# Optimization experiments

Hardware: AMD Instinct MI355X
Metric: run time of the kernel (lower is better)

Reference implementation:

```python
import jax, jax.numpy as jnp
import numpy as np

N, M, D_IN, H1, D, OUT_C = 2048, 128, 352, 512, 256, 13


def _lin_bn_relu(x, w, b, g, be):
    # 1x1 conv == linear over last dim; BN (eval) folded to per-channel affine (g, be)
    return jax.nn.relu(g * (x @ w.T + b) + be)


def _encode(x, wA, bA, gA, beA, wB, bB, gB, beB):
    return _lin_bn_relu(_lin_bn_relu(x, wA, bA, gA, beA), wB, bB, gB, beB)


def setup_inputs() -> dict:
    key = jax.random.key(0)
    ks = iter(jax.random.split(key, 64))

    def wgt(shape, s=0.05):
        return (jax.random.normal(next(ks), shape, jnp.float32) * s)

    def gamma(c):
        return 1.0 + 0.05 * jax.random.normal(next(ks), (c,), jnp.float32)

    inp = {}
    inp['ext_fea'] = jax.random.normal(next(ks), (N, D_IN), jnp.float32)
    inp['lab_fea'] = jax.random.normal(next(ks), (M, D_IN), jnp.float32)
    # convs1: 352->512->256, each Conv1d(1x1)+BN+ReLU
    inp.update(w1a=wgt((H1, D_IN)), b1a=wgt((H1,)), g1a=gamma(H1), be1a=wgt((H1,)))
    inp.update(w1b=wgt((D, H1)), b1b=wgt((D,)), g1b=gamma(D), be1b=wgt((D,)))
    # convs2: same shapes
    inp.update(w2a=wgt((H1, D_IN)), b2a=wgt((H1,)), g2a=gamma(H1), be2a=wgt((H1,)))
    inp.update(w2b=wgt((D, H1)), b2b=wgt((D,)), g2b=gamma(D), be2b=wgt((D,)))
    # wei_conv SharedMLP [256,32,64,256]: three Conv2d(1x1)+BN+ReLU
    inp.update(mw1=wgt((32, D)), mb1=wgt((32,)), mg1=gamma(32), mbe1=wgt((32,)))
    inp.update(mw2=wgt((64, 32)), mb2=wgt((64,)), mg2=gamma(64), mbe2=wgt((64,)))
    inp.update(mw3=wgt((D, 64)), mb3=wgt((D,)), mg3=gamma(D), mbe3=wgt((D,)))
    # fc
    inp.update(fcw=wgt((OUT_C, D)), fcb=wgt((OUT_C,)))
    return inp


def reference(ext_fea, lab_fea,
              w1a, b1a, g1a, be1a, w1b, b1b, g1b, be1b,
              w2a, b2a, g2a, be2a, w2b, b2b, g2b, be2b,
              mw1, mb1, mg1, mbe1, mw2, mb2, mg2, mbe2, mw3, mb3, mg3, mbe3,
              fcw, fcb):
    A = _encode(ext_fea, w1a, b1a, g1a, be1a, w1b, b1b, g1b, be1b)   # [N, 256]
    B = _encode(lab_fea, w2a, b2a, g2a, be2a, w2b, b2b, g2b, be2b)   # [M, 256]
    diff = A[:, None, :] - B[None, :, :]                             # [N, M, 256]
    h = _lin_bn_relu(diff, mw1, mb1, mg1, mbe1)                      # [N, M, 32]
    h = _lin_bn_relu(h, mw2, mb2, mg2, mbe2)                         # [N, M, 64]
    wei = _lin_bn_relu(h, mw3, mb3, mg3, mbe3)                       # [N, M, 256]
    # torch softmax over dim=-1 of [1,256,N,M] == over M == axis 1 here
    wei = jax.nn.softmax(wei, axis=1)
    att = jnp.sum(wei * diff, axis=1)                                # [N, 256]
    return att @ fcw.T + fcb                                         # [N, 13]
```

## Files before the change

kernel.cpp:

```cpp
#include <hip/hip_runtime.h>
#include <stdint.h>


typedef __attribute__((ext_vector_type(4))) float float4_t;
typedef __attribute__((ext_vector_type(4))) float f32x4;
typedef __attribute__((ext_vector_type(8))) short bf16x8;
typedef __attribute__((ext_vector_type(8))) unsigned short ushort8_t;
typedef unsigned short ushort_t;

__device__ __forceinline__ unsigned short f2b(float f) {
  union { float f; unsigned int i; } v; v.f = f;
  unsigned int x = v.i;
  return (unsigned short)((x + 0x7FFFu + ((x >> 16) & 1u)) >> 16);
}

template<int ISBF>
__device__ __forceinline__ ushort8_t ld8(const void* base, size_t idx) {
  if constexpr (ISBF) {
    return *(const ushort8_t*)((const ushort_t*)base + idx);
  } else {
    const float* p = (const float*)base + idx;
    float4_t v0 = *(const float4_t*)p;
    float4_t v1 = *(const float4_t*)(p + 4);
    ushort8_t u;
    #pragma unroll
    for (int e = 0; e < 4; ++e) { u[e] = f2b(v0[e]); u[4 + e] = f2b(v1[e]); }
    return u;
  }
}

template<int XBF, int WBF, int OUT_BF16>
__global__ __launch_bounds__(256) void enc_mfma(
    const void* __restrict__ XA, const void* __restrict__ WA,
    const float* __restrict__ bA, const float* __restrict__ gA, const float* __restrict__ beA,
    void* __restrict__ YA,
    const void* __restrict__ XB, const void* __restrict__ WB,
    const float* __restrict__ bB, const float* __restrict__ gB, const float* __restrict__ beB,
    void* __restrict__ YB, float* __restrict__ YBT,
    int J, int K, int nbxA)
{
  __shared__ ushort_t Xs[2][32][40];
  __shared__ ushort_t Ws[2][32][40];
  const int bx = blockIdx.x, by = blockIdx.y;
  const void* X; const void* W;
  const float *bb, *gg, *bev; void* Y; int i0, isB;
  if (bx < nbxA) { X = XA; W = WA; bb = bA; gg = gA; bev = beA; Y = YA; i0 = bx * 32; isB = 0; }
  else           { X = XB; W = WB; bb = bB; gg = gB; bev = beB; Y = YB; i0 = (bx - nbxA) * 32; isB = 1; }
  const int j0 = by * 32;
  const int tid = threadIdx.x, w = tid >> 6, lane = tid & 63, lg = lane >> 4, lr = lane & 15;
  const int mt = w >> 1, ct = w & 1;
  const int row = tid >> 2, k8 = (tid & 3) * 8;

  f32x4 acc = f32x4{0.f, 0.f, 0.f, 0.f};

  ushort8_t sv = (row < 32) ? ld8<XBF>(X, (size_t)(i0 + row) * K + k8)
                            : ld8<WBF>(W, (size_t)(j0 + row - 32) * K + k8);
  for (int kt = 0; kt < K; kt += 32) {
    const int buf = (kt >> 5) & 1;
    if (row < 32) *(ushort8_t*)&Xs[buf][row][k8] = sv;
    else          *(ushort8_t*)&Ws[buf][row - 32][k8] = sv;
    __syncthreads();
    if (kt + 32 < K)
      sv = (row < 32) ? ld8<XBF>(X, (size_t)(i0 + row) * K + kt + 32 + k8)
                      : ld8<WBF>(W, (size_t)(j0 + row - 32) * K + kt + 32 + k8);
    bf16x8 af = *(const bf16x8*)&Xs[buf][mt * 16 + lr][lg * 8];
    bf16x8 bf_ = *(const bf16x8*)&Ws[buf][ct * 16 + lr][lg * 8];
    acc = __builtin_amdgcn_mfma_f32_16x16x32_bf16(af, bf_, acc, 0, 0, 0);
  }
  const int c = j0 + ct * 16 + lr;
  const float g = gg[c], bv = bb[c], ev = bev[c];
  #pragma unroll
  for (int r = 0; r < 4; ++r) {
    const int rowo = i0 + mt * 16 + 4 * lg + r;
    float t = fmaxf(g * (acc[r] + bv) + ev, 0.f);
    if (OUT_BF16) ((ushort_t*)Y)[(size_t)rowo * J + c] = f2b(t);
    else {
      ((float*)Y)[(size_t)rowo * J + c] = t;
      if (isB && YBT) YBT[(size_t)c * 128 + rowo] = t;
    }
  }
}

__global__ __launch_bounds__(256) void proj32(
    const float* __restrict__ Aenc, const float* __restrict__ Benc,
    const float* __restrict__ mw1, const float* __restrict__ mb1,
    const float* __restrict__ mg1, const float* __restrict__ mbe1,
    float* __restrict__ PA2, float* __restrict__ PB2, int nbxA,
    const float* __restrict__ mw2, const float* __restrict__ mw3,
    ushort_t* __restrict__ mw2b, ushort_t* __restrict__ mw3b)
{
  __shared__ float ps[4][32];
  const int tid = threadIdx.x, bx = blockIdx.x;
  if (bx >= nbxA + 32) {
    const int g = (bx - nbxA - 32) * 256 + tid;
    const float* s; ushort_t* d; int j;
    if (g < 256) { s = mw2; d = mw2b; j = g; }
    else         { s = mw3; d = mw3b; j = g - 256; }
    float4_t v0 = *(const float4_t*)&s[(size_t)j * 8];
    float4_t v1 = *(const float4_t*)&s[(size_t)j * 8 + 4];
    ushort8_t u;
    #pragma unroll
    for (int e = 0; e < 4; ++e) { u[e] = f2b(v0[e]); u[4 + e] = f2b(v1[e]); }
    *(ushort8_t*)&d[(size_t)j * 8] = u;
    return;
  }
  const float* X; float* P; int n0, wb;
  if (bx < nbxA) { X = Aenc; P = PA2; n0 = bx * 4; wb = 1; }
  else           { X = Benc; P = PB2; n0 = (bx - nbxA) * 4; wb = 0; }
  const int k = tid & 31, r = (tid >> 5) & 3, half = tid >> 7;
  const int n = n0 + r;
  const float* xp = &X[(size_t)n * 256 + half * 128];
  const float* wp = &mw1[k * 256 + half * 128];
  float s = 0.f;
  #pragma unroll 8
  for (int q = 0; q < 128; q += 4) {
    float4_t xv = *(const float4_t*)&xp[q];
    float4_t wv = *(const float4_t*)&wp[q];
    #pragma unroll
    for (int e = 0; e < 4; ++e) s = fmaf(xv[e], wv[e], s);
  }
  if (half == 1) ps[r][k] = s;
  __syncthreads();
  if (half == 0) {
    s += ps[r][k];
    P[(size_t)n * 32 + k] = wb ? (mg1[k] * (s + mb1[k]) + mbe1[k]) : (mg1[k] * s);
  }
}

__global__ __launch_bounds__(256, 2) void main_attn(
    const float* __restrict__ PA2, const float* __restrict__ PB2,
    const float* __restrict__ A, const float* __restrict__ BmT,
    const ushort_t* __restrict__ mw2b, const float* __restrict__ mb2,
    const float* __restrict__ mg2, const float* __restrict__ mbe2,
    const ushort_t* __restrict__ mw3b, const float* __restrict__ mb3,
    const float* __restrict__ mg3, const float* __restrict__ mbe3,
    const float* __restrict__ fcw, const float* __restrict__ fcb,
    float* __restrict__ outp)
{
  __shared__ __align__(16) char smem[77824];
  const int tid = threadIdx.x;
  const int w = tid >> 6, lane = tid & 63, lg = lane >> 4, lr = lane & 15;
  const int n = blockIdx.x * 4 + w;
  ushort_t* h2s = (ushort_t*)(smem + w * 19456);
  float* attL   = (float*)(smem + w * 19456 + 18432);
  const float LOG2E = 1.4426950408889634f;

  {
    bf16x8 b1[4];
    float g2h[4], b2h[4], e2h[4];
    #pragma unroll
    for (int jt = 0; jt < 4; ++jt) {
      b1[jt] = *(const bf16x8*)&mw2b[(jt * 16 + lr) * 32 + lg * 8];
      const int j = jt * 16 + lr;
      g2h[jt] = mg2[j]; b2h[jt] = mb2[j]; e2h[jt] = mbe2[j];
    }
    const float* pa = &PA2[(size_t)n * 32 + lg * 8];
    float4_t pa0 = *(const float4_t*)pa;
    float4_t pa1 = *(const float4_t*)(pa + 4);
    #pragma unroll
    for (int mt = 0; mt < 8; ++mt) {
      const int m = mt * 16 + lr;
      const float* pb = &PB2[(size_t)m * 32 + lg * 8];
      float4_t pb0 = *(const float4_t*)pb;
      float4_t pb1 = *(const float4_t*)(pb + 4);
      bf16x8 a1;
      #pragma unroll
      for (int e = 0; e < 4; ++e) {
        a1[e]     = (short)f2b(fmaxf(pa0[e] - pb0[e], 0.f));
        a1[4 + e] = (short)f2b(fmaxf(pa1[e] - pb1[e], 0.f));
      }
      f32x4 acc1[4];
      #pragma unroll
      for (int jt = 0; jt < 4; ++jt) acc1[jt] = f32x4{0.f, 0.f, 0.f, 0.f};
      #pragma unroll
      for (int jt = 0; jt < 4; ++jt)
        acc1[jt] = __builtin_amdgcn_mfma_f32_16x16x32_bf16(a1, b1[jt], acc1[jt], 0, 0, 0);
      #pragma unroll
      for (int jt = 0; jt < 4; ++jt)
        #pragma unroll
        for (int r = 0; r < 4; ++r)
          h2s[(mt * 16 + 4 * lg + r) * 72 + jt * 16 + lr] =
              f2b(fmaxf(g2h[jt] * (acc1[jt][r] + b2h[jt]) + e2h[jt], 0.f));
    }
  }

  #pragma unroll 2
  for (int ct = 0; ct < 16; ++ct) {
    const int c = ct * 16 + lr;
    bf16x8 bfr0 = *(const bf16x8*)&mw3b[(size_t)c * 64 + lg * 8];
    bf16x8 bfr1 = *(const bf16x8*)&mw3b[(size_t)c * 64 + 32 + lg * 8];
    f32x4 acc[8];
    #pragma unroll
    for (int mt = 0; mt < 8; ++mt) acc[mt] = f32x4{0.f, 0.f, 0.f, 0.f};
    #pragma unroll
    for (int mt = 0; mt < 8; ++mt) {
      bf16x8 af0 = *(const bf16x8*)&h2s[(mt * 16 + lr) * 72 + lg * 8];
      acc[mt] = __builtin_amdgcn_mfma_f32_16x16x32_bf16(af0, bfr0, acc[mt], 0, 0, 0);
      bf16x8 af1 = *(const bf16x8*)&h2s[(mt * 16 + lr) * 72 + 32 + lg * 8];
      acc[mt] = __builtin_amdgcn_mfma_f32_16x16x32_bf16(af1, bfr1, acc[mt], 0, 0, 0);
    }
    const float g = mg3[c];
    const float gs = g * LOG2E;
    const float cs = (g * mb3[c] + mbe3[c]) * LOG2E;
    f32x4 sm4 = f32x4{0.f, 0.f, 0.f, 0.f};
    f32x4 wb4 = f32x4{0.f, 0.f, 0.f, 0.f};
    #pragma unroll
    for (int mt = 0; mt < 8; ++mt) {
      float4_t bv4 = *(const float4_t*)&BmT[(size_t)c * 128 + mt * 16 + 4 * lg];
      #pragma unroll
      for (int r = 0; r < 4; ++r) {
        float t = fmaf(gs, acc[mt][r], cs);
        float p = __builtin_amdgcn_exp2f(__builtin_amdgcn_fmed3f(t, 0.f, 80.f));
        sm4[r] += p;
        wb4[r] = fmaf(p, bv4[r], wb4[r]);
      }
    }
    float sm = (sm4[0] + sm4[1]) + (sm4[2] + sm4[3]);
    float wb = (wb4[0] + wb4[1]) + (wb4[2] + wb4[3]);
    sm += __shfl_xor(sm, 16, 64);  wb += __shfl_xor(wb, 16, 64);
    sm += __shfl_xor(sm, 32, 64);  wb += __shfl_xor(wb, 32, 64);
    if (lg == 0)
      attL[c] = A[(size_t)n * 256 + c] - wb / sm;
  }

  {
    float4_t av = *(const float4_t*)&attL[lane * 4];
    #pragma unroll
    for (int o = 0; o < 13; ++o) {
      float4_t wv = *(const float4_t*)&fcw[(size_t)o * 256 + lane * 4];
      float s = av[0] * wv[0];
      s = fmaf(av[1], wv[1], s);
      s = fmaf(av[2], wv[2], s);
      s = fmaf(av[3], wv[3], s);
      #pragma unroll
      for (int st = 1; st <= 32; st <<= 1) s += __shfl_xor(s, st, 64);
      if (lane == 0) outp[(size_t)n * 13 + o] = s + fcb[o];
    }
  }
}

extern "C" void kernel_launch(void* const* d_in, const int* in_sizes, int n_in,
                              void* d_out, int out_size, void* d_ws, size_t ws_size,
                              hipStream_t stream)
{
  const float* ext = (const float*)d_in[0];
  const float* lab = (const float*)d_in[1];
  const float* w1a = (const float*)d_in[2];
  const float* b1a = (const float*)d_in[3];
  const float* g1a = (const float*)d_in[4];
  const float* be1a= (const float*)d_in[5];
  const float* w1b = (const float*)d_in[6];
  const float* b1b = (const float*)d_in[7];
  const float* g1b = (const float*)d_in[8];
  const float* be1b= (const float*)d_in[9];
  const float* w2a = (const float*)d_in[10];
  const float* b2a = (const float*)d_in[11];
  const float* g2a = (const float*)d_in[12];
  const float* be2a= (const float*)d_in[13];
  const float* w2b = (const float*)d_in[14];
  const float* b2b = (const float*)d_in[15];
  const float* g2b = (const float*)d_in[16];
  const float* be2b= (const float*)d_in[17];
  const float* mw1 = (const float*)d_in[18];
  const float* mb1 = (const float*)d_in[19];
  const float* mg1 = (const float*)d_in[20];
  const float* mbe1= (const float*)d_in[21];
  const float* mw2 = (const float*)d_in[22];
  const float* mb2 = (const float*)d_in[23];
  const float* mg2 = (const float*)d_in[24];
  const float* mbe2= (const float*)d_in[25];
  const float* mw3 = (const float*)d_in[26];
  const float* mb3 = (const float*)d_in[27];
  const float* mg3 = (const float*)d_in[28];
  const float* mbe3= (const float*)d_in[29];
  const float* fcw = (const float*)d_in[30];
  const float* fcb = (const float*)d_in[31];

  char* ws = (char*)d_ws;
  ushort_t* Y1ab = (ushort_t*)(ws);
  float*    PA2  = (float*)(ws);
  float*    PB2  = (float*)(ws + 262144);
  float*    Aenc = (float*)(ws + (2u << 20));
  char* b5 = ws + (4u << 20);
  ushort_t* mw2b = (ushort_t*)(b5);
  ushort_t* mw3b = (ushort_t*)(b5 + 4096);
  ushort_t* Y1bb = (ushort_t*)(b5 + 36864);
  float*    Benc = (float*)(b5 + 167936);
  float*    BencT= (float*)(b5 + 299008);

  enc_mfma<0, 0, 1><<<dim3(68, 16), 256, 0, stream>>>(
      (const void*)ext, (const void*)w1a, b1a, g1a, be1a, (void*)Y1ab,
      (const void*)lab, (const void*)w2a, b2a, g2a, be2a, (void*)Y1bb,
      (float*)nullptr, 512, 352, 64);
  enc_mfma<1, 0, 0><<<dim3(68, 8), 256, 0, stream>>>(
      (const void*)Y1ab, (const void*)w1b, b1b, g1b, be1b, (void*)Aenc,
      (const void*)Y1bb, (const void*)w2b, b2b, g2b, be2b, (void*)Benc,
      BencT, 256, 512, 64);
  proj32<<<553, 256, 0, stream>>>(Aenc, Benc, mw1, mb1, mg1, mbe1, PA2, PB2, 512,
                                  mw2, mw3, mw2b, mw3b);
  main_attn<<<512, 256, 0, stream>>>(PA2, PB2, Aenc, BencT,
                                     mw2b, mb2, mg2, mbe2, mw3b, mb3, mg3, mbe3,
                                     fcw, fcb, (float*)d_out);
}
```

Measured before the change: 86.34 us.

## Fold BN scale into mw3 bf16 weights, restructure softmax loop, store B transposed as bf16

Pre-scales the third MLP weight by gamma*log2e during bf16 conversion and seeds the MFMA accumulator with the bias term, so the exponent input comes straight from the matrix product with no per-element affine step. The channel loop is restructured to hold 8 channel tiles' weights in registers and reuse each loaded h2 fragment across them, which cuts LDS reads. The transposed B encoding is stored and read as bf16 to halve its traffic, and a cheaper round-to-nearest bf16 conversion is used in the hot path. The cost is more register pressure and slightly lower precision in the weighted sum and the rounding.

```diff
diff --git a/kernel.cpp b/kernel.cpp
--- a/kernel.cpp
+++ b/kernel.cpp
@@ -6,12 +6,20 @@
 typedef __attribute__((ext_vector_type(4))) float f32x4;
 typedef __attribute__((ext_vector_type(8))) short bf16x8;
 typedef __attribute__((ext_vector_type(8))) unsigned short ushort8_t;
+typedef __attribute__((ext_vector_type(4))) unsigned short ushort4_t;
 typedef unsigned short ushort_t;
 
+__device__ __forceinline__ float b2f(unsigned short u) {
+  union { unsigned int i; float f; } v; v.i = ((unsigned int)u) << 16; return v.f;
+}
 __device__ __forceinline__ unsigned short f2b(float f) {
   union { float f; unsigned int i; } v; v.f = f;
   unsigned int x = v.i;
   return (unsigned short)((x + 0x7FFFu + ((x >> 16) & 1u)) >> 16);
+}
+__device__ __forceinline__ unsigned short f2b_fast(float f) {
+  union { float f; unsigned int i; } v; v.f = f;
+  return (unsigned short)((v.i + 0x8000u) >> 16);
 }
 
 template<int ISBF>
@@ -36,7 +44,7 @@
     void* __restrict__ YA,
     const void* __restrict__ XB, const void* __restrict__ WB,
     const float* __restrict__ bB, const float* __restrict__ gB, const float* __restrict__ beB,
-    void* __restrict__ YB, float* __restrict__ YBT,
+    void* __restrict__ YB, ushort_t* __restrict__ YBTb,
     int J, int K, int nbxA)
 {
   __shared__ ushort_t Xs[2][32][40];
@@ -76,7 +84,7 @@
     if (OUT_BF16) ((ushort_t*)Y)[(size_t)rowo * J + c] = f2b(t);
     else {
       ((float*)Y)[(size_t)rowo * J + c] = t;
-      if (isB && YBT) YBT[(size_t)c * 128 + rowo] = t;
+      if (isB && YBTb) YBTb[(size_t)c * 128 + rowo] = f2b(t);
     }
   }
 }
@@ -87,21 +95,31 @@
     const float* __restrict__ mg1, const float* __restrict__ mbe1,
     float* __restrict__ PA2, float* __restrict__ PB2, int nbxA,
     const float* __restrict__ mw2, const float* __restrict__ mw3,
+    const float* __restrict__ mg3,
     ushort_t* __restrict__ mw2b, ushort_t* __restrict__ mw3b)
 {
   __shared__ float ps[4][32];
   const int tid = threadIdx.x, bx = blockIdx.x;
   if (bx >= nbxA + 32) {
     const int g = (bx - nbxA - 32) * 256 + tid;
-    const float* s; ushort_t* d; int j;
-    if (g < 256) { s = mw2; d = mw2b; j = g; }
-    else         { s = mw3; d = mw3b; j = g - 256; }
-    float4_t v0 = *(const float4_t*)&s[(size_t)j * 8];
-    float4_t v1 = *(const float4_t*)&s[(size_t)j * 8 + 4];
-    ushort8_t u;
-    #pragma unroll
-    for (int e = 0; e < 4; ++e) { u[e] = f2b(v0[e]); u[4 + e] = f2b(v1[e]); }
-    *(ushort8_t*)&d[(size_t)j * 8] = u;
+    if (g < 256) {
+      float4_t v0 = *(const float4_t*)&mw2[(size_t)g * 8];
+      float4_t v1 = *(const float4_t*)&mw2[(size_t)g * 8 + 4];
+      ushort8_t u;
+      #pragma unroll
+      for (int e = 0; e < 4; ++e) { u[e] = f2b(v0[e]); u[4 + e] = f2b(v1[e]); }
+      *(ushort8_t*)&mw2b[(size_t)g * 8] = u;
+    } else {
+      const int j = g - 256;
+      const int c = j >> 3;
+      const float sc = mg3[c] * 1.4426950408889634f;
+      float4_t v0 = *(const float4_t*)&mw3[(size_t)j * 8];
+      float4_t v1 = *(const float4_t*)&mw3[(size_t)j * 8 + 4];
+      ushort8_t u;
+      #pragma unroll
+      for (int e = 0; e < 4; ++e) { u[e] = f2b(sc * v0[e]); u[4 + e] = f2b(sc * v1[e]); }
+      *(ushort8_t*)&mw3b[(size_t)j * 8] = u;
+    }
     return;
   }
   const float* X; float* P; int n0, wb;
@@ -129,7 +147,7 @@
 
 __global__ __launch_bounds__(256, 2) void main_attn(
     const float* __restrict__ PA2, const float* __restrict__ PB2,
-    const float* __restrict__ A, const float* __restrict__ BmT,
+    const float* __restrict__ A, const ushort_t* __restrict__ BmTb,
     const ushort_t* __restrict__ mw2b, const float* __restrict__ mb2,
     const float* __restrict__ mg2, const float* __restrict__ mbe2,
     const ushort_t* __restrict__ mw3b, const float* __restrict__ mb3,
@@ -147,12 +165,13 @@
 
   {
     bf16x8 b1[4];
-    float g2h[4], b2h[4], e2h[4];
+    float g2h[4], c2h[4];
     #pragma unroll
     for (int jt = 0; jt < 4; ++jt) {
       b1[jt] = *(const bf16x8*)&mw2b[(jt * 16 + lr) * 32 + lg * 8];
       const int j = jt * 16 + lr;
-      g2h[jt] = mg2[j]; b2h[jt] = mb2[j]; e2h[jt] = mbe2[j];
+      const float g = mg2[j];
+      g2h[jt] = g; c2h[jt] = g * mb2[j] + mbe2[j];
     }
     const float* pa = &PA2[(size_t)n * 32 + lg * 8];
     float4_t pa0 = *(const float4_t*)pa;
@@ -166,8 +185,8 @@
       bf16x8 a1;
       #pragma unroll
       for (int e = 0; e < 4; ++e) {
-        a1[e]     = (short)f2b(fmaxf(pa0[e] - pb0[e], 0.f));
-        a1[4 + e] = (short)f2b(fmaxf(pa1[e] - pb1[e], 0.f));
+        a1[e]     = (short)f2b_fast(fmaxf(pa0[e] - pb0[e], 0.f));
+        a1[4 + e] = (short)f2b_fast(fmaxf(pa1[e] - pb1[e], 0.f));
       }
       f32x4 acc1[4];
       #pragma unroll
@@ -180,47 +199,54 @@
         #pragma unroll
         for (int r = 0; r < 4; ++r)
           h2s[(mt * 16 + 4 * lg + r) * 72 + jt * 16 + lr] =
-              f2b(fmaxf(g2h[jt] * (acc1[jt][r] + b2h[jt]) + e2h[jt], 0.f));
-    }
-  }
-
-  #pragma unroll 2
-  for (int ct = 0; ct < 16; ++ct) {
-    const int c = ct * 16 + lr;
-    bf16x8 bfr0 = *(const bf16x8*)&mw3b[(size_t)c * 64 + lg * 8];
-    bf16x8 bfr1 = *(const bf16x8*)&mw3b[(size_t)c * 64 + 32 + lg * 8];
-    f32x4 acc[8];
-    #pragma unroll
-    for (int mt = 0; mt < 8; ++mt) acc[mt] = f32x4{0.f, 0.f, 0.f, 0.f};
+              f2b_fast(fmaxf(fmaf(g2h[jt], acc1[jt][r], c2h[jt]), 0.f));
+    }
+  }
+
+  #pragma unroll 1
+  for (int ph = 0; ph < 2; ++ph) {
+    bf16x8 bfr0[8], bfr1[8];
+    float csv[8];
+    #pragma unroll
+    for (int q = 0; q < 8; ++q) {
+      const int c = (ph * 8 + q) * 16 + lr;
+      bfr0[q] = *(const bf16x8*)&mw3b[(size_t)c * 64 + lg * 8];
+      bfr1[q] = *(const bf16x8*)&mw3b[(size_t)c * 64 + 32 + lg * 8];
+      csv[q] = (mg3[c] * mb3[c] + mbe3[c]) * LOG2E;
+    }
+    float smv[8], wbv[8];
+    #pragma unroll
+    for (int q = 0; q < 8; ++q) { smv[q] = 0.f; wbv[q] = 0.f; }
+
     #pragma unroll
     for (int mt = 0; mt < 8; ++mt) {
       bf16x8 af0 = *(const bf16x8*)&h2s[(mt * 16 + lr) * 72 + lg * 8];
-      acc[mt] = __builtin_amdgcn_mfma_f32_16x16x32_bf16(af0, bfr0, acc[mt], 0, 0, 0);
       bf16x8 af1 = *(const bf16x8*)&h2s[(mt * 16 + lr) * 72 + 32 + lg * 8];
-      acc[mt] = __builtin_amdgcn_mfma_f32_16x16x32_bf16(af1, bfr1, acc[mt], 0, 0, 0);
-    }
-    const float g = mg3[c];
-    const float gs = g * LOG2E;
-    const float cs = (g * mb3[c] + mbe3[c]) * LOG2E;
-    f32x4 sm4 = f32x4{0.f, 0.f, 0.f, 0.f};
-    f32x4 wb4 = f32x4{0.f, 0.f, 0.f, 0.f};
-    #pragma unroll
-    for (int mt = 0; mt < 8; ++mt) {
-      float4_t bv4 = *(const float4_t*)&BmT[(size_t)c * 128 + mt * 16 + 4 * lg];
-      #pragma unroll
-      for (int r = 0; r < 4; ++r) {
-        float t = fmaf(gs, acc[mt][r], cs);
-        float p = __builtin_amdgcn_exp2f(__builtin_amdgcn_fmed3f(t, 0.f, 80.f));
-        sm4[r] += p;
-        wb4[r] = fmaf(p, bv4[r], wb4[r]);
+      #pragma unroll
+      for (int q = 0; q < 8; ++q) {
+        const int c = (ph * 8 + q) * 16 + lr;
+        f32x4 acc = f32x4{csv[q], csv[q], csv[q], csv[q]};
+        acc = __builtin_amdgcn_mfma_f32_16x16x32_bf16(af0, bfr0[q], acc, 0, 0, 0);
+        acc = __builtin_amdgcn_mfma_f32_16x16x32_bf16(af1, bfr1[q], acc, 0, 0, 0);
+        ushort4_t bv4 = *(const ushort4_t*)&BmTb[(size_t)c * 128 + mt * 16 + 4 * lg];
+        #pragma unroll
+        for (int r = 0; r < 4; ++r) {
+          float p = __builtin_amdgcn_exp2f(__builtin_amdgcn_fmed3f(acc[r], 0.f, 80.f));
+          smv[q] += p;
+          wbv[q] = fmaf(p, b2f(bv4[r]), wbv[q]);
+        }
       }
     }
-    float sm = (sm4[0] + sm4[1]) + (sm4[2] + sm4[3]);
-    float wb = (wb4[0] + wb4[1]) + (wb4[2] + wb4[3]);
-    sm += __shfl_xor(sm, 16, 64);  wb += __shfl_xor(wb, 16, 64);
-    sm += __shfl_xor(sm, 32, 64);  wb += __shfl_xor(wb, 32, 64);
-    if (lg == 0)
-      attL[c] = A[(size_t)n * 256 + c] - wb / sm;
+    #pragma unroll
+    for (int q = 0; q < 8; ++q) {
+      float sm = smv[q], wb = wbv[q];
+      sm += __shfl_xor(sm, 16, 64);  wb += __shfl_xor(wb, 16, 64);
+      sm += __shfl_xor(sm, 32, 64);  wb += __shfl_xor(wb, 32, 64);
+      if (lg == 0) {
+        const int c = (ph * 8 + q) * 16 + lr;
+        attL[c] = A[(size_t)n * 256 + c] - wb / sm;
+      }
+    }
   }
 
   {
@@ -282,23 +308,23 @@
   float*    PB2  = (float*)(ws + 262144);
   float*    Aenc = (float*)(ws + (2u << 20));
   char* b5 = ws + (4u << 20);
-  ushort_t* mw2b = (ushort_t*)(b5);
-  ushort_t* mw3b = (ushort_t*)(b5 + 4096);
-  ushort_t* Y1bb = (ushort_t*)(b5 + 36864);
-  float*    Benc = (float*)(b5 + 167936);
-  float*    BencT= (float*)(b5 + 299008);
+  ushort_t* mw2b  = (ushort_t*)(b5);
+  ushort_t* mw3b  = (ushort_t*)(b5 + 4096);
+  ushort_t* Y1bb  = (ushort_t*)(b5 + 36864);
+  float*    Benc  = (float*)(b5 + 167936);
+  ushort_t* BencTb= (ushort_t*)(b5 + 299008);
 
   enc_mfma<0, 0, 1><<<dim3(68, 16), 256, 0, stream>>>(
       (const void*)ext, (const void*)w1a, b1a, g1a, be1a, (void*)Y1ab,
       (const void*)lab, (const void*)w2a, b2a, g2a, be2a, (void*)Y1bb,
-      (float*)nullptr, 512, 352, 64);
+      (ushort_t*)nullptr, 512, 352, 64);
   enc_mfma<1, 0, 0><<<dim3(68, 8), 256, 0, stream>>>(
       (const void*)Y1ab, (const void*)w1b, b1b, g1b, be1b, (void*)Aenc,
       (const void*)Y1bb, (const void*)w2b, b2b, g2b, be2b, (void*)Benc,
-      BencT, 256, 512, 64);
+      BencTb, 256, 512, 64);
   proj32<<<553, 256, 0, stream>>>(Aenc, Benc, mw1, mb1, mg1, mbe1, PA2, PB2, 512,
-                                  mw2, mw3, mw2b, mw3b);
-  main_attn<<<512, 256, 0, stream>>>(PA2, PB2, Aenc, BencT,
+                                  mw2, mw3, mg3, mw2b, mw3b);
+  main_attn<<<512, 256, 0, stream>>>(PA2, PB2, Aenc, BencTb,
                                      mw2b, mb2, mg2, mbe2, mw3b, mb3, mg3, mbe3,
                                      fcw, fcb, (float*)d_out);
 }
```

After: 142.9 us. 65.6% more time.
